# Kernel tuning notes

Measured on AMD Instinct MI355X. Metric: run time of the kernel, lower is better.

The kernel has to match this reference:

```python
import jax, jax.numpy as jnp
import numpy as np

B, S, D = 128, 50, 128
NUM_NODE = 40000
SAMPLE = 12
HOP = 2
ALPHA = 0.2  # leaky-relu slope (opt.alpha)


def _leaky(x, slope=ALPHA):
    return jnp.where(x >= 0, x, slope * x)


def setup_inputs() -> dict:
    key = jax.random.key(0)
    ks = jax.random.split(key, 12)
    stdv = 1.0 / float(np.sqrt(D))
    inputs = jax.random.randint(ks[0], (B, S), 0, NUM_NODE)
    adj = jax.random.randint(ks[1], (B, S, S), 0, 5)
    mask_item = jax.random.randint(ks[2], (B, S), 0, 2).at[:, 0].set(1)
    item = jax.random.randint(ks[3], (B, S), 0, NUM_NODE)
    adj_all = jax.random.randint(ks[4], (NUM_NODE, SAMPLE), 0, NUM_NODE)
    num_weight = jax.random.uniform(ks[5], (NUM_NODE, SAMPLE), dtype=jnp.float32)
    embedding = jax.random.uniform(ks[6], (NUM_NODE, D), minval=-stdv, maxval=stdv, dtype=jnp.float32)
    a_local = jax.random.uniform(ks[7], (4, D), minval=-stdv, maxval=stdv, dtype=jnp.float32)
    agg_w1 = jax.random.uniform(ks[8], (HOP, D + 1, D), minval=-stdv, maxval=stdv, dtype=jnp.float32)
    agg_w2 = jax.random.uniform(ks[9], (HOP, D, 1), minval=-stdv, maxval=stdv, dtype=jnp.float32)
    agg_w3 = jax.random.uniform(ks[10], (HOP, 2 * D, D), minval=-stdv, maxval=stdv, dtype=jnp.float32)
    return dict(inputs=inputs, adj=adj, mask_item=mask_item, item=item,
                adj_all=adj_all, num_weight=num_weight, embedding=embedding,
                a_local=a_local, agg_w1=agg_w1, agg_w2=agg_w2, agg_w3=agg_w3)


def _local_agg(h, adj, a_local):
    # e_k[b,i,j] = leakyrelu(sum_d h[b,i,d]*h[b,j,d]*a_k[d]); never materialize [B,N,N,D]
    e = _leaky(jnp.einsum('bid,bjd,kd->kbij', h, h, a_local))  # [4,B,S,S]
    alpha = jnp.full(e.shape[1:], -9e15, dtype=h.dtype)
    for k in range(4):
        alpha = jnp.where(adj == k + 1, e[k], alpha)
    alpha = jax.nn.softmax(alpha, axis=-1)
    return alpha @ h


def _global_agg(w1, w2, w3, self_v, neigh_v, neigh_w, extra):
    # self_v [B,L,D]; neigh_v [B,L,SAMPLE,D]; neigh_w [B,L,SAMPLE]; extra [B,L,D]
    feat = jnp.concatenate([extra[:, :, None, :] * neigh_v, neigh_w[..., None]], axis=-1)  # [B,L,SAMPLE,D+1]
    a = _leaky(feat @ w1, 0.2)                              # [B,L,SAMPLE,D]
    a = jax.nn.softmax((a @ w2)[..., 0], axis=-1)[..., None]  # [B,L,SAMPLE,1]
    neigh = jnp.sum(a * neigh_v, axis=-2)                   # [B,L,D]
    out = jnp.concatenate([self_v, neigh], axis=-1) @ w3    # [B,L,D]
    return jax.nn.relu(out)


def _forward(inputs, adj, mask_item, item, adj_all, num_weight, embedding,
             a_local, agg_w1, agg_w2, agg_w3):
    h = embedding[inputs]                          # [B,S,D]
    h_local = _local_agg(h, adj, a_local)
    # multi-hop neighbor sampling (index_select into adj_all / num)
    item_neighbors = [inputs]
    weight_neighbors = []
    support = S
    for _ in range(HOP):
        last = item_neighbors[-1].reshape(-1)
        support *= SAMPLE
        item_neighbors.append(adj_all[last].reshape(B, support))
        weight_neighbors.append(num_weight[last].reshape(B, support))
    entity = [embedding[idx] for idx in item_neighbors]
    mask_f = mask_item.astype(h.dtype)
    item_emb = embedding[item] * mask_f[..., None]
    session = (jnp.sum(item_emb, 1) / jnp.sum(mask_f, -1, keepdims=True))[:, None, :]  # [B,1,D]
    for n_hop in range(HOP):
        nxt = []
        for hop in range(HOP - n_hop):
            self_v = entity[hop]
            L = self_v.shape[1]
            neigh_v = entity[hop + 1].reshape(B, L, SAMPLE, D)
            neigh_w = weight_neighbors[hop].reshape(B, L, SAMPLE)
            extra = jnp.broadcast_to(session, (B, L, D))
            nxt.append(_global_agg(agg_w1[n_hop], agg_w2[n_hop], agg_w3[n_hop],
                                   self_v, neigh_v, neigh_w, extra))
        entity = nxt
    h_global = entity[0].reshape(B, S, D)
    # dropout_local / dropout_global are identity in eval mode
    return h_local + h_global


def reference(inputs, adj, mask_item, item, adj_all, num_weight, embedding,
              a_local, agg_w1, agg_w2, agg_w3):
    return _forward(inputs, adj, mask_item, item, adj_all, num_weight, embedding,
                    a_local, agg_w1, agg_w2, agg_w3)
```

## Files before the change

kernel.cpp:

```cpp
#include <hip/hip_runtime.h>
#include <math.h>

#define BATCH 128
#define S 50
#define D 128
#define SAMPLE 12

typedef __attribute__((ext_vector_type(8))) short short8v;
typedef __attribute__((ext_vector_type(4))) float f32x4;
typedef unsigned short u16;

__device__ __forceinline__ float leakyf(float x) { return x >= 0.f ? x : 0.2f * x; }
__device__ __forceinline__ u16 f2bf(float f) {
    union { float f; unsigned u; } v; v.f = f;
    unsigned u = v.u;
    return (u16)((u + 0x7FFFu + ((u >> 16) & 1u)) >> 16);
}
__device__ __forceinline__ float bf2f(u16 h) {
    union { float f; unsigned u; } v; v.u = ((unsigned)h) << 16; return v.f;
}

__global__ __launch_bounds__(256) void setup_kernel(
    const int* __restrict__ item, const int* __restrict__ mask,
    const int* __restrict__ inputs, const int* __restrict__ adj_all,
    const float* __restrict__ emb, float* __restrict__ session, int* __restrict__ n1)
{
    const int bx = blockIdx.x, t = threadIdx.x;
    if (bx < BATCH) {
        if (t < 128) {
            float num = 0.f, den = 0.f;
            for (int s = 0; s < S; ++s) {
                float m = (float)mask[bx * S + s];
                num += m * emb[item[bx * S + s] * D + t];
                den += m;
            }
            session[bx * D + t] = num / den;
        }
    } else {
        int idx = (bx - BATCH) * 256 + t;
        if (idx < BATCH * 600) {
            int b = idx / 600, j = idx % 600;
            n1[idx] = adj_all[inputs[b * S + j / SAMPLE] * SAMPLE + j % SAMPLE];
        }
    }
}

__global__ __launch_bounds__(256) void prep_kernel(
    const float* __restrict__ emb, const float* __restrict__ w1,
    const float* __restrict__ w3, const float* __restrict__ session,
    u16* __restrict__ emb_bf, u16* __restrict__ sw1, u16* __restrict__ w3t)
{
    const int bx = blockIdx.x, t = threadIdx.x;
    if (bx < 2500) {
        int idx = bx * 256 + t;
        const float4* src = reinterpret_cast<const float4*>(emb) + (size_t)idx * 2;
        float4 a = src[0], c = src[1];
        u16 o[8] = {f2bf(a.x), f2bf(a.y), f2bf(a.z), f2bf(a.w),
                    f2bf(c.x), f2bf(c.y), f2bf(c.z), f2bf(c.w)};
        *reinterpret_cast<uint4*>(emb_bf + (size_t)idx * 8) = *reinterpret_cast<uint4*>(o);
    } else if (bx < 2756) {
        int id = bx - 2500, hop = id >> 7, b = id & 127;
        const float* w1s = w1 + hop * 129 * 128;
        const float* se = session + b * 128;
        int n = t >> 1, kh = (t & 1) * 64;
        u16* dst = sw1 + (((size_t)(hop * 128 + b) * 128 + n) * 128) + kh;
        for (int kq = 0; kq < 64; kq += 8) {
            u16 o[8];
            #pragma unroll
            for (int e = 0; e < 8; ++e) { int k = kh + kq + e; o[e] = f2bf(w1s[k * 128 + n] * se[k]); }
            *reinterpret_cast<uint4*>(dst + kq) = *reinterpret_cast<uint4*>(o);
        }
    } else {
        int j = (bx - 2756) * 256 + t;
        int hop = j >> 12, r = j & 4095, n = r >> 5, k0 = (r & 31) * 8;
        const float* w3s = w3 + hop * 256 * 128;
        u16 o[8];
        #pragma unroll
        for (int e = 0; e < 8; ++e) o[e] = f2bf(w3s[(k0 + e) * 128 + n]);
        *reinterpret_cast<uint4*>(w3t + ((size_t)hop * 128 + n) * 256 + k0) = *reinterpret_cast<uint4*>(o);
    }
}

template <int PATH>
__global__ __launch_bounds__(256, 4) void main_kernel(
    const int* __restrict__ inputs, const int* __restrict__ adj,
    const int* __restrict__ adj_all, const float* __restrict__ num_weight,
    const float* __restrict__ emb, const float* __restrict__ a_local,
    const int* __restrict__ n1,
    const u16* __restrict__ emb_bf, const u16* __restrict__ sw1,
    const float* __restrict__ w1, const float* __restrict__ w2,
    const u16* __restrict__ w3t,
    const u16* __restrict__ in0, const u16* __restrict__ in1,
    u16* __restrict__ o0, u16* __restrict__ o1, float* __restrict__ outf)
{
    __shared__ __align__(16) char smem[37664];
    const int b = blockIdx.y;
    const int t = threadIdx.x;
    const int bx = blockIdx.x;

    if (PATH == 0 && bx == 82) {
        float (*h)[D]     = (float(*)[D])smem;
        float (*al)[D]    = (float(*)[D])(smem + 25600);
        float (*alpha)[S] = (float(*)[S])(smem + 27648);

        for (int idx = t; idx < S * D; idx += 256) {
            int i = idx / D, d = idx % D;
            h[i][d] = emb[inputs[b * S + i] * D + d];
        }
        for (int idx = t; idx < 4 * D; idx += 256) al[idx / D][idx % D] = a_local[idx];
        __syncthreads();

        for (int p = t; p < S * S; p += 256) {
            int i = p / S, j = p % S;
            int a = adj[b * S * S + p];
            float v = -9e15f;
            if (a >= 1 && a <= 4) {
                const float* ak = al[a - 1];
                float dot = 0.f;
                #pragma unroll 4
                for (int d = 0; d < D; ++d) dot += h[i][d] * h[j][d] * ak[d];
                v = leakyf(dot);
            }
            alpha[i][j] = v;
        }
        __syncthreads();

        if (t < S) {
            float m = -INFINITY;
            for (int j = 0; j < S; ++j) m = fmaxf(m, alpha[t][j]);
            float ssum = 0.f;
            for (int j = 0; j < S; ++j) { float e = expf(alpha[t][j] - m); alpha[t][j] = e; ssum += e; }
            float inv = 1.f / ssum;
            for (int j = 0; j < S; ++j) alpha[t][j] *= inv;
        }
        __syncthreads();

        for (int idx = t; idx < S * D; idx += 256) {
            int i = idx / D, d = idx % D;
            float acc = 0.f;
            #pragma unroll 5
            for (int j = 0; j < S; ++j) acc += alpha[i][j] * h[j][d];
            outf[b * S * D + idx] = acc;
        }
        return;
    }

    int mode, l0, L, hop;
    const u16 *nsrc, *ssrc;
    u16* outb;
    if (PATH == 2)      { mode = 2; l0 = bx * 8;        L = 50;  nsrc = in1;    ssrc = in0;    outb = nullptr; hop = 1; }
    else if (bx < 75)   { mode = 1; l0 = bx * 8;        L = 600; nsrc = emb_bf; ssrc = emb_bf; outb = o1;      hop = 0; }
    else                { mode = 0; l0 = (bx - 75) * 8; L = 50;  nsrc = emb_bf; ssrc = emb_bf; outb = o0;      hop = 0; }

    u16* nvL = (u16*)smem;
    u16* A2  = (u16*)(smem + 24576);
    float (*score_w)[96] = (float(*)[96])(smem + 32768);
    float* score    = (float*)(smem + 34304);
    float* nwgt     = (float*)(smem + 34688);
    int*   neighIdx = (int*)(smem + 35072);
    int*   selfNode = (int*)(smem + 35456);

    const u16*   sw1b   = sw1 + (size_t)(hop * 128 + b) * 16384;
    const float* w1last = w1 + hop * 129 * 128 + 128 * 128;
    const float* w2h    = w2 + hop * 128;
    const u16*   w3th   = w3t + hop * 32768;

    const int lane = t & 63, wv = t >> 6, cn = lane & 15, cg = lane >> 4;

    if (t < 8) {
        int l = l0 + t;
        selfNode[t] = (l < L) ? ((mode == 1) ? n1[b * 600 + l] : inputs[b * S + l]) : -1;
    }
    __syncthreads();

    if (t < 96) {
        int li = t / SAMPLE, s2 = t % SAMPLE;
        int node = selfNode[li];
        int row = -1; float wgt = 0.f;
        if (node >= 0) {
            if (mode == 0)      row = n1[b * 600 + (l0 + li) * SAMPLE + s2];
            else if (mode == 1) row = adj_all[node * SAMPLE + s2];
            else                row = b * 600 + (l0 + li) * SAMPLE + s2;
            wgt = num_weight[node * SAMPLE + s2];
        }
        neighIdx[t] = row; nwgt[t] = wgt;
    }
    *reinterpret_cast<uint4*>((char*)A2 + 8 * 512 + t * 16) = make_uint4(0, 0, 0, 0);
    __syncthreads();

    #pragma unroll
    for (int i = 0; i < 6; ++i) {
        int q = i * 256 + t;
        int m = q >> 4, dq = q & 15;
        int row = neighIdx[m];
        uint4 v = make_uint4(0, 0, 0, 0);
        if (row >= 0) v = *reinterpret_cast<const uint4*>(nsrc + (size_t)row * 128 + dq * 8);
        *reinterpret_cast<uint4*>((char*)nvL + m * 256 + ((dq * 16) ^ ((m & 7) << 4))) = v;
    }
    if (t < 128) {
        int li = t >> 4, dq = t & 15;
        int l = l0 + li;
        uint4 v = make_uint4(0, 0, 0, 0);
        if (l < L) {
            int srow = (mode == 2) ? (b * 50 + l) : selfNode[li];
            v = *reinterpret_cast<const uint4*>(ssrc + (size_t)srow * 128 + dq * 8);
        }
        *reinterpret_cast<uint4*>((char*)A2 + li * 512 + ((dq * 16) ^ ((li & 7) << 4))) = v;
    }
    __syncthreads();

    f32x4 acc[6][2];
    #pragma unroll
    for (int mt = 0; mt < 6; ++mt) {
        acc[mt][0] = (f32x4){0.f, 0.f, 0.f, 0.f};
        acc[mt][1] = (f32x4){0.f, 0.f, 0.f, 0.f};
    }
    #pragma unroll
    for (int kk = 0; kk < 4; ++kk) {
        int kbase = kk * 32 + cg * 8;
        short8v b0 = *reinterpret_cast<const short8v*>(sw1b + ((2 * wv) * 16 + cn) * 128 + kbase);
        short8v b1 = *reinterpret_cast<const short8v*>(sw1b + ((2 * wv + 1) * 16 + cn) * 128 + kbase);
        #pragma unroll
        for (int mt = 0; mt < 6; ++mt) {
            short8v a = *reinterpret_cast<const short8v*>(
                (const char*)nvL + (mt * 16 + cn) * 256 + ((kbase * 2) ^ ((cn & 7) << 4)));
            acc[mt][0] = __builtin_amdgcn_mfma_f32_16x16x32_bf16(a, b0, acc[mt][0], 0, 0, 0);
            acc[mt][1] = __builtin_amdgcn_mfma_f32_16x16x32_bf16(a, b1, acc[mt][1], 0, 0, 0);
        }
    }

    {
        float w2v0 = w2h[(2 * wv) * 16 + cn];
        float w2v1 = w2h[(2 * wv + 1) * 16 + cn];
        float w1l0 = w1last[(2 * wv) * 16 + cn];
        float w1l1 = w1last[(2 * wv + 1) * 16 + cn];
        #pragma unroll
        for (int mt = 0; mt < 6; ++mt) {
            #pragma unroll
            for (int r = 0; r < 4; ++r) {
                float nw = nwgt[mt * 16 + cg * 4 + r];
                float v = leakyf(acc[mt][0][r] + nw * w1l0) * w2v0 +
                          leakyf(acc[mt][1][r] + nw * w1l1) * w2v1;
                v += __shfl_xor(v, 1); v += __shfl_xor(v, 2);
                v += __shfl_xor(v, 4); v += __shfl_xor(v, 8);
                if (cn == 0) score_w[wv][mt * 16 + cg * 4 + r] = v;
            }
        }
    }
    __syncthreads();

    if (t < 8) {
        float e[SAMPLE]; float mx = -INFINITY;
        #pragma unroll
        for (int s2 = 0; s2 < SAMPLE; ++s2) {
            int m = t * SAMPLE + s2;
            float v = score_w[0][m] + score_w[1][m] + score_w[2][m] + score_w[3][m];
            e[s2] = v; mx = fmaxf(mx, v);
        }
        float ssum = 0.f;
        #pragma unroll
        for (int s2 = 0; s2 < SAMPLE; ++s2) { e[s2] = expf(e[s2] - mx); ssum += e[s2]; }
        float inv = 1.f / ssum;
        #pragma unroll
        for (int s2 = 0; s2 < SAMPLE; ++s2) score[t * SAMPLE + s2] = e[s2] * inv;
    }
    __syncthreads();

    #pragma unroll
    for (int i = 0; i < 2; ++i) {
        int idx = i * 256 + t;
        int l = idx >> 6, d2 = idx & 63;
        float a0 = 0.f, a1 = 0.f;
        #pragma unroll
        for (int s2 = 0; s2 < SAMPLE; ++s2) {
            int m = l * SAMPLE + s2;
            unsigned pk = *reinterpret_cast<const unsigned*>(
                (const char*)nvL + m * 256 + ((4 * d2) ^ ((m & 7) << 4)));
            float sc = score[m];
            a0 += sc * bf2f((u16)(pk & 0xffff));
            a1 += sc * bf2f((u16)(pk >> 16));
        }
        unsigned packed = ((unsigned)f2bf(a1) << 16) | f2bf(a0);
        *reinterpret_cast<unsigned*>((char*)A2 + l * 512 + ((256 + 4 * d2) ^ ((l & 7) << 4))) = packed;
    }
    __syncthreads();

    f32x4 acc2[2];
    acc2[0] = (f32x4){0.f, 0.f, 0.f, 0.f};
    acc2[1] = (f32x4){0.f, 0.f, 0.f, 0.f};
    #pragma unroll
    for (int kk = 0; kk < 8; ++kk) {
        int kbase = kk * 32 + cg * 8;
        short8v a = *reinterpret_cast<const short8v*>(
            (const char*)A2 + cn * 512 + ((kbase * 2) ^ ((cn & 7) << 4)));
        short8v bb0 = *reinterpret_cast<const short8v*>(w3th + ((2 * wv) * 16 + cn) * 256 + kbase);
        short8v bb1 = *reinterpret_cast<const short8v*>(w3th + ((2 * wv + 1) * 16 + cn) * 256 + kbase);
        acc2[0] = __builtin_amdgcn_mfma_f32_16x16x32_bf16(a, bb0, acc2[0], 0, 0, 0);
        acc2[1] = __builtin_amdgcn_mfma_f32_16x16x32_bf16(a, bb1, acc2[1], 0, 0, 0);
    }
    #pragma unroll
    for (int j = 0; j < 2; ++j) {
        int n = (2 * wv + j) * 16 + cn;
        #pragma unroll
        for (int r = 0; r < 4; ++r) {
            int rowi = cg * 4 + r;
            if (rowi < 8 && (l0 + rowi) < L) {
                float val = fmaxf(acc2[j][r], 0.f);
                if (PATH == 2) {
                    float* p = outf + ((size_t)(b * 50) + l0 + rowi) * 128 + n;
                    *p = val + *p;
                } else {
                    outb[((size_t)b * L + l0 + rowi) * 128 + n] = f2bf(val);
                }
            }
        }
    }
}

extern "C" void kernel_launch(void* const* d_in, const int* in_sizes, int n_in,
                              void* d_out, int out_size, void* d_ws, size_t ws_size,
                              hipStream_t stream)
{
    const int*   inputs     = (const int*)d_in[0];
    const int*   adj        = (const int*)d_in[1];
    const int*   mask_item  = (const int*)d_in[2];
    const int*   item       = (const int*)d_in[3];
    const int*   adj_all    = (const int*)d_in[4];
    const float* num_weight = (const float*)d_in[5];
    const float* embedding  = (const float*)d_in[6];
    const float* a_local    = (const float*)d_in[7];
    const float* agg_w1     = (const float*)d_in[8];
    const float* agg_w2     = (const float*)d_in[9];
    const float* agg_w3     = (const float*)d_in[10];
    float* out = (float*)d_out;

    char* w = (char*)d_ws;
    float* ws_session = (float*)(w);
    int*   ws_n1      = (int*)(w + 65536);
    u16*   ws_emb     = (u16*)(w + 372736);
    u16*   ws_sw1     = (u16*)(w + 10612736);
    u16*   ws_w3t     = (u16*)(w + 19001344);
    u16*   ws_out0    = (u16*)(w + 19132416);
    u16*   ws_out1    = (u16*)(w + 20770816);

    setup_kernel<<<dim3(BATCH + 300), 256, 0, stream>>>(
        item, mask_item, inputs, adj_all, embedding, ws_session, ws_n1);
    prep_kernel<<<dim3(2788), 256, 0, stream>>>(
        embedding, agg_w1, agg_w3, ws_session, ws_emb, ws_sw1, ws_w3t);

    main_kernel<0><<<dim3(83, BATCH), 256, 0, stream>>>(
        inputs, adj, adj_all, num_weight, embedding, a_local, ws_n1,
        ws_emb, ws_sw1, agg_w1, agg_w2, ws_w3t,
        nullptr, nullptr, ws_out0, ws_out1, out);

    main_kernel<2><<<dim3(7, BATCH), 256, 0, stream>>>(
        inputs, adj, adj_all, num_weight, embedding, a_local, ws_n1,
        ws_emb, ws_sw1, agg_w1, agg_w2, ws_w3t,
        ws_out0, ws_out1, nullptr, nullptr, out);
}
```

Measured before the change: 330.4 us.

## Precompute hop-2 neighbor tables and reassociate W3 matmul before score-weighted sum

Neighbor indices and weights for both hops are now precomputed in the setup and prep kernels, so the main kernel no longer chases adj_all chains with extra syncs. LDS tiles are stored in MFMA-fragment order instead of swizzled rows. The final aggregation multiplies every neighbor by the W3 neighbor half with MFMA first and then applies the softmax scores in registers, which removes one LDS pass and one barrier. The cost is more MFMA work and extra global workspace traffic for the n2 and nw1 tables.

```diff
diff --git a/kernel.cpp b/kernel.cpp
--- a/kernel.cpp
+++ b/kernel.cpp
@@ -20,10 +20,11 @@
     union { float f; unsigned u; } v; v.u = ((unsigned)h) << 16; return v.f;
 }
 
-__global__ __launch_bounds__(256) void setup_kernel(
+__global__ __launch_bounds__(256) void setup1_kernel(
     const int* __restrict__ item, const int* __restrict__ mask,
     const int* __restrict__ inputs, const int* __restrict__ adj_all,
-    const float* __restrict__ emb, float* __restrict__ session, int* __restrict__ n1)
+    const float* __restrict__ num_weight, const float* __restrict__ emb,
+    float* __restrict__ session, int* __restrict__ n1, float* __restrict__ nw0)
 {
     const int bx = blockIdx.x, t = threadIdx.x;
     if (bx < BATCH) {
@@ -40,15 +41,20 @@
         int idx = (bx - BATCH) * 256 + t;
         if (idx < BATCH * 600) {
             int b = idx / 600, j = idx % 600;
-            n1[idx] = adj_all[inputs[b * S + j / SAMPLE] * SAMPLE + j % SAMPLE];
-        }
-    }
-}
-
-__global__ __launch_bounds__(256) void prep_kernel(
+            int node = inputs[b * S + j / SAMPLE];
+            n1[idx]  = adj_all[node * SAMPLE + j % SAMPLE];
+            nw0[idx] = num_weight[node * SAMPLE + j % SAMPLE];
+        }
+    }
+}
+
+__global__ __launch_bounds__(256) void prep2_kernel(
     const float* __restrict__ emb, const float* __restrict__ w1,
     const float* __restrict__ w3, const float* __restrict__ session,
-    u16* __restrict__ emb_bf, u16* __restrict__ sw1, u16* __restrict__ w3t)
+    const int* __restrict__ adj_all, const float* __restrict__ num_weight,
+    const int* __restrict__ n1,
+    u16* __restrict__ emb_bf, u16* __restrict__ sw1, u16* __restrict__ w3t,
+    int* __restrict__ n2, float* __restrict__ nw1)
 {
     const int bx = blockIdx.x, t = threadIdx.x;
     if (bx < 2500) {
@@ -70,7 +76,7 @@
             for (int e = 0; e < 8; ++e) { int k = kh + kq + e; o[e] = f2bf(w1s[k * 128 + n] * se[k]); }
             *reinterpret_cast<uint4*>(dst + kq) = *reinterpret_cast<uint4*>(o);
         }
-    } else {
+    } else if (bx < 2788) {
         int j = (bx - 2756) * 256 + t;
         int hop = j >> 12, r = j & 4095, n = r >> 5, k0 = (r & 31) * 8;
         const float* w3s = w3 + hop * 256 * 128;
@@ -78,15 +84,23 @@
         #pragma unroll
         for (int e = 0; e < 8; ++e) o[e] = f2bf(w3s[(k0 + e) * 128 + n]);
         *reinterpret_cast<uint4*>(w3t + ((size_t)hop * 128 + n) * 256 + k0) = *reinterpret_cast<uint4*>(o);
+    } else {
+        int idx = (bx - 2788) * 256 + t;
+        if (idx < BATCH * 7200) {
+            int b = idx / 7200, j = idx % 7200;
+            int node = n1[b * 600 + j / SAMPLE];
+            n2[idx]  = adj_all[node * SAMPLE + j % SAMPLE];
+            nw1[idx] = num_weight[node * SAMPLE + j % SAMPLE];
+        }
     }
 }
 
 template <int PATH>
 __global__ __launch_bounds__(256, 4) void main_kernel(
     const int* __restrict__ inputs, const int* __restrict__ adj,
-    const int* __restrict__ adj_all, const float* __restrict__ num_weight,
     const float* __restrict__ emb, const float* __restrict__ a_local,
-    const int* __restrict__ n1,
+    const int* __restrict__ n1, const int* __restrict__ n2,
+    const float* __restrict__ nw0, const float* __restrict__ nw1,
     const u16* __restrict__ emb_bf, const u16* __restrict__ sw1,
     const float* __restrict__ w1, const float* __restrict__ w2,
     const u16* __restrict__ w3t,
@@ -145,20 +159,19 @@
         return;
     }
 
-    int mode, l0, L, hop;
+    int mode, l0, L, Lm, hop;
     const u16 *nsrc, *ssrc;
+    const int* idxTab; const float* nwTab;
     u16* outb;
-    if (PATH == 2)      { mode = 2; l0 = bx * 8;        L = 50;  nsrc = in1;    ssrc = in0;    outb = nullptr; hop = 1; }
-    else if (bx < 75)   { mode = 1; l0 = bx * 8;        L = 600; nsrc = emb_bf; ssrc = emb_bf; outb = o1;      hop = 0; }
-    else                { mode = 0; l0 = (bx - 75) * 8; L = 50;  nsrc = emb_bf; ssrc = emb_bf; outb = o0;      hop = 0; }
-
-    u16* nvL = (u16*)smem;
-    u16* A2  = (u16*)(smem + 24576);
-    float (*score_w)[96] = (float(*)[96])(smem + 32768);
-    float* score    = (float*)(smem + 34304);
-    float* nwgt     = (float*)(smem + 34688);
-    int*   neighIdx = (int*)(smem + 35072);
-    int*   selfNode = (int*)(smem + 35456);
+    if (PATH == 2)    { mode = 2; l0 = bx * 8;        L = 50;  Lm = 600;  nsrc = in1;    ssrc = in0;    idxTab = nullptr; nwTab = nw0; outb = nullptr; hop = 1; }
+    else if (bx < 75) { mode = 1; l0 = bx * 8;        L = 600; Lm = 7200; nsrc = emb_bf; ssrc = emb_bf; idxTab = n2;      nwTab = nw1; outb = o1;      hop = 0; }
+    else              { mode = 0; l0 = (bx - 75) * 8; L = 50;  Lm = 600;  nsrc = emb_bf; ssrc = emb_bf; idxTab = n1;      nwTab = nw0; outb = o0;      hop = 0; }
+
+    u16* nvL   = (u16*)smem;
+    u16* selfL = (u16*)(smem + 24576);
+    float (*score_w)[96] = (float(*)[96])(smem + 28672);
+    float* score = (float*)(smem + 30208);
+    float* nwgtL = (float*)(smem + 30592);
 
     const u16*   sw1b   = sw1 + (size_t)(hop * 128 + b) * 16384;
     const float* w1last = w1 + hop * 129 * 128 + 128 * 128;
@@ -166,46 +179,33 @@
     const u16*   w3th   = w3t + hop * 32768;
 
     const int lane = t & 63, wv = t >> 6, cn = lane & 15, cg = lane >> 4;
-
-    if (t < 8) {
-        int l = l0 + t;
-        selfNode[t] = (l < L) ? ((mode == 1) ? n1[b * 600 + l] : inputs[b * S + l]) : -1;
-    }
-    __syncthreads();
-
+    const int nc0 = (2 * wv) * 16 + cn, nc1 = (2 * wv + 1) * 16 + cn;
+
+    #pragma unroll
+    for (int i = 0; i < 6; ++i) {
+        int slot = i * 256 + t;
+        int mt = slot >> 8, kk = (slot >> 6) & 3;
+        int ln2 = slot & 63, cg2 = ln2 >> 4, cn2 = ln2 & 15;
+        int gm = l0 * 12 + (cn2 >> 2) * 24 + mt * 4 + (cn2 & 3);
+        int gmc = (gm < Lm) ? gm : 0;
+        int row = (PATH == 2) ? (b * 600 + gmc) : idxTab[b * Lm + gmc];
+        int chunk = kk * 4 + cg2;
+        uint4 v = *reinterpret_cast<const uint4*>(nsrc + (size_t)row * 128 + chunk * 8);
+        *reinterpret_cast<uint4*>(nvL + slot * 8) = v;
+    }
+    {
+        int kk = t >> 6, ln2 = t & 63, cg2 = ln2 >> 4, i2 = ln2 & 15;
+        int l = 2 * (i2 >> 2) + ((i2 >> 1) & 1);
+        int lg = l0 + l; if (lg >= L) lg = 0;
+        int srow;
+        if (PATH == 2) srow = b * 50 + lg;
+        else           srow = (mode == 1) ? n1[b * 600 + lg] : inputs[b * S + lg];
+        uint4 v = *reinterpret_cast<const uint4*>(ssrc + (size_t)srow * 128 + (kk * 4 + cg2) * 8);
+        *reinterpret_cast<uint4*>(selfL + t * 8) = v;
+    }
     if (t < 96) {
-        int li = t / SAMPLE, s2 = t % SAMPLE;
-        int node = selfNode[li];
-        int row = -1; float wgt = 0.f;
-        if (node >= 0) {
-            if (mode == 0)      row = n1[b * 600 + (l0 + li) * SAMPLE + s2];
-            else if (mode == 1) row = adj_all[node * SAMPLE + s2];
-            else                row = b * 600 + (l0 + li) * SAMPLE + s2;
-            wgt = num_weight[node * SAMPLE + s2];
-        }
-        neighIdx[t] = row; nwgt[t] = wgt;
-    }
-    *reinterpret_cast<uint4*>((char*)A2 + 8 * 512 + t * 16) = make_uint4(0, 0, 0, 0);
-    __syncthreads();
-
-    #pragma unroll
-    for (int i = 0; i < 6; ++i) {
-        int q = i * 256 + t;
-        int m = q >> 4, dq = q & 15;
-        int row = neighIdx[m];
-        uint4 v = make_uint4(0, 0, 0, 0);
-        if (row >= 0) v = *reinterpret_cast<const uint4*>(nsrc + (size_t)row * 128 + dq * 8);
-        *reinterpret_cast<uint4*>((char*)nvL + m * 256 + ((dq * 16) ^ ((m & 7) << 4))) = v;
-    }
-    if (t < 128) {
-        int li = t >> 4, dq = t & 15;
-        int l = l0 + li;
-        uint4 v = make_uint4(0, 0, 0, 0);
-        if (l < L) {
-            int srow = (mode == 2) ? (b * 50 + l) : selfNode[li];
-            v = *reinterpret_cast<const uint4*>(ssrc + (size_t)srow * 128 + dq * 8);
-        }
-        *reinterpret_cast<uint4*>((char*)A2 + li * 512 + ((dq * 16) ^ ((li & 7) << 4))) = v;
+        int gm = l0 * 12 + t;
+        nwgtL[t] = (gm < Lm) ? nwTab[b * Lm + gm] : 0.f;
     }
     __syncthreads();
 
@@ -217,33 +217,31 @@
     }
     #pragma unroll
     for (int kk = 0; kk < 4; ++kk) {
-        int kbase = kk * 32 + cg * 8;
-        short8v b0 = *reinterpret_cast<const short8v*>(sw1b + ((2 * wv) * 16 + cn) * 128 + kbase);
-        short8v b1 = *reinterpret_cast<const short8v*>(sw1b + ((2 * wv + 1) * 16 + cn) * 128 + kbase);
+        int kb = kk * 32 + cg * 8;
+        short8v b0 = *reinterpret_cast<const short8v*>(sw1b + nc0 * 128 + kb);
+        short8v b1 = *reinterpret_cast<const short8v*>(sw1b + nc1 * 128 + kb);
         #pragma unroll
         for (int mt = 0; mt < 6; ++mt) {
-            short8v a = *reinterpret_cast<const short8v*>(
-                (const char*)nvL + (mt * 16 + cn) * 256 + ((kbase * 2) ^ ((cn & 7) << 4)));
+            short8v a = *reinterpret_cast<const short8v*>(nvL + ((mt * 4 + kk) * 64 + lane) * 8);
             acc[mt][0] = __builtin_amdgcn_mfma_f32_16x16x32_bf16(a, b0, acc[mt][0], 0, 0, 0);
             acc[mt][1] = __builtin_amdgcn_mfma_f32_16x16x32_bf16(a, b1, acc[mt][1], 0, 0, 0);
         }
     }
 
     {
-        float w2v0 = w2h[(2 * wv) * 16 + cn];
-        float w2v1 = w2h[(2 * wv + 1) * 16 + cn];
-        float w1l0 = w1last[(2 * wv) * 16 + cn];
-        float w1l1 = w1last[(2 * wv + 1) * 16 + cn];
+        float w2v0 = w2h[nc0], w2v1 = w2h[nc1];
+        float w1l0 = w1last[nc0], w1l1 = w1last[nc1];
         #pragma unroll
         for (int mt = 0; mt < 6; ++mt) {
             #pragma unroll
             for (int r = 0; r < 4; ++r) {
-                float nw = nwgt[mt * 16 + cg * 4 + r];
+                int m = cg * 24 + mt * 4 + r;
+                float nw = nwgtL[m];
                 float v = leakyf(acc[mt][0][r] + nw * w1l0) * w2v0 +
                           leakyf(acc[mt][1][r] + nw * w1l1) * w2v1;
                 v += __shfl_xor(v, 1); v += __shfl_xor(v, 2);
                 v += __shfl_xor(v, 4); v += __shfl_xor(v, 8);
-                if (cn == 0) score_w[wv][mt * 16 + cg * 4 + r] = v;
+                if (cn == 0) score_w[wv][m] = v;
             }
         }
     }
@@ -266,52 +264,63 @@
     }
     __syncthreads();
 
-    #pragma unroll
-    for (int i = 0; i < 2; ++i) {
-        int idx = i * 256 + t;
-        int l = idx >> 6, d2 = idx & 63;
-        float a0 = 0.f, a1 = 0.f;
-        #pragma unroll
-        for (int s2 = 0; s2 < SAMPLE; ++s2) {
-            int m = l * SAMPLE + s2;
-            unsigned pk = *reinterpret_cast<const unsigned*>(
-                (const char*)nvL + m * 256 + ((4 * d2) ^ ((m & 7) << 4)));
-            float sc = score[m];
-            a0 += sc * bf2f((u16)(pk & 0xffff));
-            a1 += sc * bf2f((u16)(pk >> 16));
-        }
-        unsigned packed = ((unsigned)f2bf(a1) << 16) | f2bf(a0);
-        *reinterpret_cast<unsigned*>((char*)A2 + l * 512 + ((256 + 4 * d2) ^ ((l & 7) << 4))) = packed;
-    }
-    __syncthreads();
-
-    f32x4 acc2[2];
-    acc2[0] = (f32x4){0.f, 0.f, 0.f, 0.f};
-    acc2[1] = (f32x4){0.f, 0.f, 0.f, 0.f};
-    #pragma unroll
-    for (int kk = 0; kk < 8; ++kk) {
-        int kbase = kk * 32 + cg * 8;
-        short8v a = *reinterpret_cast<const short8v*>(
-            (const char*)A2 + cn * 512 + ((kbase * 2) ^ ((cn & 7) << 4)));
-        short8v bb0 = *reinterpret_cast<const short8v*>(w3th + ((2 * wv) * 16 + cn) * 256 + kbase);
-        short8v bb1 = *reinterpret_cast<const short8v*>(w3th + ((2 * wv + 1) * 16 + cn) * 256 + kbase);
-        acc2[0] = __builtin_amdgcn_mfma_f32_16x16x32_bf16(a, bb0, acc2[0], 0, 0, 0);
-        acc2[1] = __builtin_amdgcn_mfma_f32_16x16x32_bf16(a, bb1, acc2[1], 0, 0, 0);
-    }
-    #pragma unroll
-    for (int j = 0; j < 2; ++j) {
-        int n = (2 * wv + j) * 16 + cn;
+    f32x4 accS0 = (f32x4){0.f, 0.f, 0.f, 0.f};
+    f32x4 accS1 = (f32x4){0.f, 0.f, 0.f, 0.f};
+    #pragma unroll
+    for (int mt = 0; mt < 6; ++mt) {
+        acc[mt][0] = (f32x4){0.f, 0.f, 0.f, 0.f};
+        acc[mt][1] = (f32x4){0.f, 0.f, 0.f, 0.f};
+    }
+    #pragma unroll
+    for (int kk = 0; kk < 4; ++kk) {
+        int kb = kk * 32 + cg * 8;
+        short8v by0 = *reinterpret_cast<const short8v*>(w3th + nc0 * 256 + 128 + kb);
+        short8v by1 = *reinterpret_cast<const short8v*>(w3th + nc1 * 256 + 128 + kb);
+        short8v bs0 = *reinterpret_cast<const short8v*>(w3th + nc0 * 256 + kb);
+        short8v bs1 = *reinterpret_cast<const short8v*>(w3th + nc1 * 256 + kb);
+        short8v aS = *reinterpret_cast<const short8v*>(selfL + (kk * 64 + lane) * 8);
+        accS0 = __builtin_amdgcn_mfma_f32_16x16x32_bf16(aS, bs0, accS0, 0, 0, 0);
+        accS1 = __builtin_amdgcn_mfma_f32_16x16x32_bf16(aS, bs1, accS1, 0, 0, 0);
+        #pragma unroll
+        for (int mt = 0; mt < 6; ++mt) {
+            short8v a = *reinterpret_cast<const short8v*>(nvL + ((mt * 4 + kk) * 64 + lane) * 8);
+            acc[mt][0] = __builtin_amdgcn_mfma_f32_16x16x32_bf16(a, by0, acc[mt][0], 0, 0, 0);
+            acc[mt][1] = __builtin_amdgcn_mfma_f32_16x16x32_bf16(a, by1, acc[mt][1], 0, 0, 0);
+        }
+    }
+    float P00 = 0.f, P01 = 0.f, P10 = 0.f, P11 = 0.f;
+    #pragma unroll
+    for (int mt = 0; mt < 6; ++mt) {
         #pragma unroll
         for (int r = 0; r < 4; ++r) {
-            int rowi = cg * 4 + r;
-            if (rowi < 8 && (l0 + rowi) < L) {
-                float val = fmaxf(acc2[j][r], 0.f);
-                if (PATH == 2) {
-                    float* p = outf + ((size_t)(b * 50) + l0 + rowi) * 128 + n;
-                    *p = val + *p;
-                } else {
-                    outb[((size_t)b * L + l0 + rowi) * 128 + n] = f2bf(val);
-                }
+            float al = score[cg * 24 + mt * 4 + r];
+            if (mt < 3) { P00 += al * acc[mt][0][r]; P01 += al * acc[mt][1][r]; }
+            else        { P10 += al * acc[mt][0][r]; P11 += al * acc[mt][1][r]; }
+        }
+    }
+    {
+        float v00 = fmaxf(P00 + accS0[0], 0.f);
+        float v01 = fmaxf(P01 + accS1[0], 0.f);
+        float v10 = fmaxf(P10 + accS0[2], 0.f);
+        float v11 = fmaxf(P11 + accS1[2], 0.f);
+        int lg0 = l0 + cg * 2, lg1 = lg0 + 1;
+        if (PATH == 2) {
+            if (lg0 < L) {
+                float* p = outf + ((size_t)b * 50 + lg0) * 128;
+                p[nc0] += v00; p[nc1] += v01;
+            }
+            if (lg1 < L) {
+                float* p = outf + ((size_t)b * 50 + lg1) * 128;
+                p[nc0] += v10; p[nc1] += v11;
+            }
+        } else {
+            if (lg0 < L) {
+                u16* p = outb + ((size_t)b * L + lg0) * 128;
+                p[nc0] = f2bf(v00); p[nc1] = f2bf(v01);
+            }
+            if (lg1 < L) {
+                u16* p = outb + ((size_t)b * L + lg1) * 128;
+                p[nc0] = f2bf(v10); p[nc1] = f2bf(v11);
             }
         }
     }
@@ -337,24 +346,29 @@
     char* w = (char*)d_ws;
     float* ws_session = (float*)(w);
     int*   ws_n1      = (int*)(w + 65536);
-    u16*   ws_emb     = (u16*)(w + 372736);
-    u16*   ws_sw1     = (u16*)(w + 10612736);
-    u16*   ws_w3t     = (u16*)(w + 19001344);
-    u16*   ws_out0    = (u16*)(w + 19132416);
-    u16*   ws_out1    = (u16*)(w + 20770816);
-
-    setup_kernel<<<dim3(BATCH + 300), 256, 0, stream>>>(
-        item, mask_item, inputs, adj_all, embedding, ws_session, ws_n1);
-    prep_kernel<<<dim3(2788), 256, 0, stream>>>(
-        embedding, agg_w1, agg_w3, ws_session, ws_emb, ws_sw1, ws_w3t);
+    float* ws_nw0     = (float*)(w + 372736);
+    int*   ws_n2      = (int*)(w + 679936);
+    float* ws_nw1     = (float*)(w + 4366336);
+    u16*   ws_emb     = (u16*)(w + 8052736);
+    u16*   ws_sw1     = (u16*)(w + 18292736);
+    u16*   ws_w3t     = (u16*)(w + 26681344);
+    u16*   ws_out0    = (u16*)(w + 26812416);
+    u16*   ws_out1    = (u16*)(w + 28450816);
+
+    setup1_kernel<<<dim3(BATCH + 300), 256, 0, stream>>>(
+        item, mask_item, inputs, adj_all, num_weight, embedding,
+        ws_session, ws_n1, ws_nw0);
+    prep2_kernel<<<dim3(6388), 256, 0, stream>>>(
+        embedding, agg_w1, agg_w3, ws_session, adj_all, num_weight, ws_n1,
+        ws_emb, ws_sw1, ws_w3t, ws_n2, ws_nw1);
 
     main_kernel<0><<<dim3(83, BATCH), 256, 0, stream>>>(
-        inputs, adj, adj_all, num_weight, embedding, a_local, ws_n1,
+        inputs, adj, embedding, a_local, ws_n1, ws_n2, ws_nw0, ws_nw1,
         ws_emb, ws_sw1, agg_w1, agg_w2, ws_w3t,
         nullptr, nullptr, ws_out0, ws_out1, out);
 
     main_kernel<2><<<dim3(7, BATCH), 256, 0, stream>>>(
-        inputs, adj, adj_all, num_weight, embedding, a_local, ws_n1,
+        inputs, adj, embedding, a_local, ws_n1, ws_n2, ws_nw0, ws_nw1,
         ws_emb, ws_sw1, agg_w1, agg_w2, ws_w3t,
         ws_out0, ws_out1, nullptr, nullptr, out);
 }
```

Result: no change. 332.0 us (+0.5%).
